# Kernel optimization log

Measured on AMD Instinct MI355X. Metric: run time of the kernel, lower is better.

Reference implementation:

```python
import jax, jax.numpy as jnp
import numpy as np

B, COND_LEN, E = 128, 256, 512   # batch, cond_len, hidden_dim (== conditioning_dim)
A, L, H = 128, 64, 8             # action_dim, num_action_steps, num_heads
STEPS = 20
HD = E // H


def setup_inputs() -> dict:
    key = jax.random.key(0)
    ks = jax.random.split(key, 16)
    def rn(k, shape, s=0.02):
        return jax.random.normal(k, shape, jnp.float32) * s
    return {
        "conditioning": jax.random.normal(ks[0], (B, COND_LEN, E), jnp.float32),
        "noise": jax.random.normal(ks[1], (B, L, A), jnp.float32),
        # time_embed: Linear(1,E) -> ReLU -> Linear(E,E)
        "t1_w": rn(ks[2], (E, 1)), "t1_b": jnp.zeros((E,), jnp.float32),
        "t2_w": rn(ks[3], (E, E)), "t2_b": jnp.zeros((E,), jnp.float32),
        # query_proj: Linear(A, E)
        "qp_w": rn(ks[4], (E, A)), "qp_b": jnp.zeros((E,), jnp.float32),
        # MultiheadAttention packed in_proj (3E, E) and out_proj (E, E)
        "in_w": rn(ks[5], (3 * E, E)), "in_b": jnp.zeros((3 * E,), jnp.float32),
        "op_w": rn(ks[6], (E, E)), "op_b": jnp.zeros((E,), jnp.float32),
        # output_proj: Linear(E, A)
        "outp_w": rn(ks[7], (A, E)), "outp_b": jnp.zeros((A,), jnp.float32),
        # ffn: Linear(A, 4A) -> ReLU -> Linear(4A, A)
        "f1_w": rn(ks[8], (4 * A, A)), "f1_b": jnp.zeros((4 * A,), jnp.float32),
        "f2_w": rn(ks[9], (A, 4 * A)), "f2_b": jnp.zeros((A,), jnp.float32),
        # LayerNorm(A)
        "ln_g": jnp.ones((A,), jnp.float32), "ln_b": jnp.zeros((A,), jnp.float32),
    }


def reference(conditioning, noise, t1_w, t1_b, t2_w, t2_b, qp_w, qp_b,
              in_w, in_b, op_w, op_b, outp_w, outp_b,
              f1_w, f1_b, f2_w, f2_b, ln_g, ln_b):
    dt = -1.0 / STEPS
    scale = 1.0 / np.sqrt(HD)
    # K/V of cross-attn depend only on conditioning -> hoist out of the loop
    # (same math as recomputing per step).
    k = (conditioning @ in_w[E:2 * E].T + in_b[E:2 * E]).reshape(B, COND_LEN, H, HD)
    v = (conditioning @ in_w[2 * E:].T + in_b[2 * E:]).reshape(B, COND_LEN, H, HD)

    def denoise(x_t, time):
        t = time[:, None]                                            # (B,1)
        t_emb = jnp.maximum(t @ t1_w.T + t1_b, 0.0) @ t2_w.T + t2_b  # (B,E)
        q_in = x_t @ qp_w.T + qp_b + t_emb[:, None, :]               # (B,L,E)
        q = (q_in @ in_w[:E].T + in_b[:E]).reshape(B, L, H, HD)
        scores = jnp.einsum('bqhd,bkhd->bhqk', q * scale, k)         # (B,H,L,COND_LEN)
        attn = jax.nn.softmax(scores, axis=-1)
        ctx = jnp.einsum('bhqk,bkhd->bqhd', attn, v).reshape(B, L, E)
        ctx = ctx @ op_w.T + op_b                                    # MHA out_proj
        v_t = ctx @ outp_w.T + outp_b                                # (B,L,A)
        h = x_t + v_t
        mu = jnp.mean(h, axis=-1, keepdims=True)
        var = jnp.mean((h - mu) ** 2, axis=-1, keepdims=True)
        hn = (h - mu) / jnp.sqrt(var + 1e-5) * ln_g + ln_b
        return hn + (jnp.maximum(hn @ f1_w.T + f1_b, 0.0) @ f2_w.T + f2_b)

    def step(carry, _):
        x_t, time = carry
        v_t = denoise(x_t, time)
        return (x_t + dt * v_t, time + dt), None

    init = (noise, jnp.ones((B,), jnp.float32))
    (x_t, _), _ = jax.lax.scan(step, init, None, length=STEPS)
    return x_t
```

## Files before the change

### kernel.cpp

```cpp
#include <hip/hip_runtime.h>

#define NB 128
#define CL 256
#define EE 512
#define AA 128
#define LL 64
#define HH 8
#define HD 64
#define NSTEPS 20
#define BLROWS (NB*LL)
#define LOG2E 1.4426950408889634f
#define QSCALE 64.0f
#define INV_QS 0.015625f

typedef __attribute__((ext_vector_type(8))) short bf16x8;
typedef __attribute__((ext_vector_type(4))) float f32x4;
typedef unsigned int u32;

union F8 { u32 u[2]; long l; };

__device__ __forceinline__ unsigned short f2bf(float f) {
    union { float f; unsigned u; } x; x.f = f;
    unsigned u = x.u;
    u += 0x7fffu + ((u >> 16) & 1u);
    return (unsigned short)(u >> 16);
}
__device__ __forceinline__ u32 pk4f8(f32x4 v) {
    u32 r = __builtin_amdgcn_cvt_pk_fp8_f32(v[0], v[1], 0, false);
    r = __builtin_amdgcn_cvt_pk_fp8_f32(v[2], v[3], r, true);
    return r;
}
__device__ __forceinline__ unsigned char f2f8(float v) {
    return (unsigned char)(__builtin_amdgcn_cvt_pk_fp8_f32(v, v, 0, false) & 0xffu);
}

__device__ __forceinline__ void async_copy16(const unsigned short* g, unsigned short* l) {
    __builtin_amdgcn_global_load_lds((const __attribute__((address_space(1))) u32*)g,
                                     (__attribute__((address_space(3))) u32*)l, 16, 0, 0);
}

#define MFMA(a,b,c)  __builtin_amdgcn_mfma_f32_16x16x32_bf16(a, b, c, 0, 0, 0)
#define MFMA8(a,b,c) __builtin_amdgcn_mfma_f32_16x16x32_fp8_fp8(a, b, c, 0, 0, 0)

__device__ __forceinline__ F8 build8(const u32* p, int kk, int srcA, int srcB, int odd) {
    u32 a0 = __shfl((int)p[2*kk],   srcA, 64);
    u32 b0 = __shfl((int)p[2*kk+1], srcA, 64);
    u32 a1 = __shfl((int)p[2*kk],   srcB, 64);
    u32 b1 = __shfl((int)p[2*kk+1], srcB, 64);
    F8 f; f.u[0] = odd ? b0 : a0; f.u[1] = odd ? b1 : a1;
    return f;
}


__global__ void cvt8_kernel(const float* __restrict__ src, unsigned short* __restrict__ dst, int n8) {
    int i = blockIdx.x*256 + threadIdx.x;
    if (i >= n8) return;
    const float* s = src + (size_t)i*8;
    f32x4 v0 = *(const f32x4*)s;
    f32x4 v1 = *(const f32x4*)(s + 4);
    bf16x8 o;
    o[0]=(short)f2bf(v0[0]); o[1]=(short)f2bf(v0[1]);
    o[2]=(short)f2bf(v0[2]); o[3]=(short)f2bf(v0[3]);
    o[4]=(short)f2bf(v1[0]); o[5]=(short)f2bf(v1[1]);
    o[6]=(short)f2bf(v1[2]); o[7]=(short)f2bf(v1[3]);
    *(bf16x8*)(dst + (size_t)i*8) = o;
}

__global__ void prep_eff_kernel(const float* __restrict__ in_w, const float* __restrict__ qp_w,
                                const float* __restrict__ outp_w, const float* __restrict__ op_w,
                                const float* __restrict__ op_b, const float* __restrict__ outp_b,
                                unsigned short* __restrict__ wq, unsigned short* __restrict__ wo,
                                float* __restrict__ bo) {
    int tid = blockIdx.x*256 + threadIdx.x;
    if (tid < 65536) {
        int n = tid >> 7, k = tid & 127;
        float s = 0.f;
        for (int e = 0; e < 512; ++e) s += in_w[(size_t)n*512 + e] * qp_w[(size_t)e*128 + k];
        wq[(size_t)n*128 + k] = f2bf(s * (0.125f * LOG2E * QSCALE));
    } else if (tid < 131072) {
        int t2 = tid - 65536; int n = t2 >> 9, k = t2 & 511;
        float s = 0.f;
        for (int e = 0; e < 512; ++e) s += outp_w[(size_t)n*512 + e] * op_w[(size_t)e*512 + k];
        wo[(size_t)n*512 + k] = f2bf(s);
    } else if (tid < 131200) {
        int n = tid - 131072;
        float s = outp_b[n];
        for (int e = 0; e < 512; ++e) s += outp_w[(size_t)n*512 + e] * op_b[e];
        bo[n] = s;
    }
}

__global__ void temb_kernel(const float* __restrict__ t1_w, const float* __restrict__ t1_b,
                            const float* __restrict__ t2_w, const float* __restrict__ t2_b,
                            float* __restrict__ temb) {
    int tid = blockIdx.x*256 + threadIdx.x;
    if (tid >= NSTEPS*512) return;
    int s = tid >> 9, e = tid & 511;
    float t = 1.0f - 0.05f * (float)s;
    float acc = t2_b[e];
    for (int i = 0; i < 512; ++i)
        acc += t2_w[(size_t)e*512 + i] * fmaxf(t * t1_w[i] + t1_b[i], 0.f);
    temb[tid] = acc;
}

__global__ void qbias_kernel(const float* __restrict__ in_w, const float* __restrict__ in_b,
                             const float* __restrict__ qp_b, const float* __restrict__ temb,
                             float* __restrict__ qbias) {
    int tid = blockIdx.x*256 + threadIdx.x;
    if (tid >= NSTEPS*512) return;
    int s = tid >> 9, n = tid & 511;
    float acc = in_b[n];
    const float* te = temb + (size_t)s*512;
    for (int e = 0; e < 512; ++e)
        acc += in_w[(size_t)n*512 + e] * (qp_b[e] + te[e]);
    qbias[tid] = acc * (0.125f * LOG2E * QSCALE);
}

__global__ __launch_bounds__(512, 8) void kv_kernel(const unsigned short* __restrict__ condb,
                                                    const unsigned short* __restrict__ wkv,
                                                    const float* __restrict__ bias,
                                                    unsigned char* __restrict__ K8,
                                                    unsigned char* __restrict__ V8) {
    __shared__ unsigned short As[128*64];
    __shared__ unsigned short Bs[128*64];
    int tid = threadIdx.x;
    int blk = blockIdx.x;
    int xcd = blk & 7, j = blk >> 3;
    int m0 = (xcd*32 + (j >> 3)) * 128;
    int n0 = (j & 7) * 128;
    int wv = tid >> 6, lane = tid & 63, r = lane & 15, q = lane >> 4;
    int srow = lane >> 3;
    int sg = (lane & 7) ^ srow;
    const unsigned short* agl = condb + (size_t)(m0 + wv*16 + srow)*512 + sg*8;
    const unsigned short* bgl = wkv   + (size_t)(n0 + wv*16 + srow)*512 + sg*8;
    f32x4 acc[8] = {};
#pragma unroll
    for (int kt = 0; kt < 8; ++kt) {
        int k0 = kt * 64;
#pragma unroll
        for (int ii = 0; ii < 2; ++ii) {
            async_copy16(agl + (size_t)(ii*8)*512 + k0, &As[(wv*16 + ii*8)*64]);
            async_copy16(bgl + (size_t)(ii*8)*512 + k0, &Bs[(wv*16 + ii*8)*64]);
        }
        __syncthreads();
#pragma unroll
        for (int kk = 0; kk < 2; ++kk) {
            int gof = ((kk*4 + q) ^ (r & 7)) * 8;
            bf16x8 a = *(const bf16x8*)&As[(wv*16 + r)*64 + gof];
#pragma unroll
            for (int t = 0; t < 8; ++t) {
                bf16x8 b = *(const bf16x8*)&Bs[(t*16 + r)*64 + gof];
                acc[t] = MFMA(a, b, acc[t]);
            }
        }
        __syncthreads();
    }
    int mbase = m0 + wv*16 + q*4;
    int bb = mbase >> 8, kpb = mbase & 255;
#pragma unroll
    for (int t = 0; t < 8; ++t) {
        int n = n0 + t*16 + r;
        float bs = bias[n];
        if (n < 512) {
            int h = n >> 6, d = n & 63;
            int colp = ((d>>3)&3)*16 + ((d>>5)&1)*8 + (d&7);
            unsigned char* kp = K8 + (size_t)(bb*HH + h)*16384 + colp;
#pragma unroll
            for (int i = 0; i < 4; ++i)
                kp[(kpb + i)*64] = f2f8(acc[t][i] + bs);
        } else {
            int n2 = n - 512, h = n2 >> 6, d = n2 & 63;
            int kk = kpb >> 5, qq = (kpb >> 3) & 3, jb = kpb & 7;
            int colv = (kk>>1)*64 + qq*16 + (kk&1)*8 + jb;
            u32 w01 = __builtin_amdgcn_cvt_pk_fp8_f32(acc[t][0]+bs, acc[t][1]+bs, 0, false);
            w01 = __builtin_amdgcn_cvt_pk_fp8_f32(acc[t][2]+bs, acc[t][3]+bs, w01, true);
            *(u32*)(V8 + (size_t)(bb*HH + h)*16384 + d*256 + colv) = w01;
        }
    }
}

__global__ __launch_bounds__(256, 2) void mega_kernel(
        const unsigned char* __restrict__ Kg,
        const unsigned char* __restrict__ Vg,
        const float* __restrict__ noise,
        const unsigned short* __restrict__ wq,
        const float* __restrict__ qbiasB,
        const unsigned short* __restrict__ wo,
        const float* __restrict__ bo,
        const float* __restrict__ ln_g, const float* __restrict__ ln_b,
        const unsigned short* __restrict__ f1w,
        const float* __restrict__ f1_b,
        const unsigned short* __restrict__ f2w,
        const float* __restrict__ f2_b,
        float* __restrict__ outp) {
    __shared__ unsigned short xS[16*136];
    __shared__ unsigned short cuS[16*520];
    __shared__ unsigned short hnS[16*136];
    __shared__ float redS[16*4], redS2[16*4];

    int tid = threadIdx.x, w = tid >> 6, lane = tid & 63, r = lane & 15, q = lane >> 4;
    int vblk = ((blockIdx.x & 7) << 6) | (blockIdx.x >> 3);
    int b = vblk >> 2;
    int row0 = vblk * 16;
    int srcA = r + ((2*q) & 3)*16;
    int srcB = r + ((2*q + 1) & 3)*16;
    int odd = (q >> 1) & 1;

    float xf[2][4];
#pragma unroll
    for (int t = 0; t < 2; ++t)
#pragma unroll
        for (int i = 0; i < 4; ++i) {
            int rl = q*4 + i, col = w*32 + t*16 + r;
            float v = noise[(size_t)(row0 + rl)*AA + col];
            xf[t][i] = v;
            xS[rl*136 + col] = f2bf(v);
        }
    __syncthreads();

    const float dt = -1.f / (float)NSTEPS;

#pragma unroll 1
    for (int s = 0; s < NSTEPS; ++s) {
        const float* qb_s = qbiasB + (size_t)s*512;

#pragma unroll 1
        for (int hp = 0; hp < 2; ++hp) {
            int h = w*2 + hp;
            const unsigned char* kbase = Kg + ((size_t)b*HH + h)*16384;
            const unsigned char* vbase = Vg + ((size_t)b*HH + h)*16384;

            f32x4 qacc[4] = {};
#pragma unroll
            for (int kk = 0; kk < 4; ++kk) {
                bf16x8 bx = *(const bf16x8*)&xS[(r)*136 + kk*32 + q*8];
#pragma unroll
                for (int t = 0; t < 4; ++t) {
                    bf16x8 a = *(const bf16x8*)(wq + (size_t)(h*HD + t*16 + r)*AA + kk*32 + q*8);
                    qacc[t] = MFMA(a, bx, qacc[t]);
                }
            }
            u32 qp[4];
#pragma unroll
            for (int t = 0; t < 4; ++t) {
                f32x4 qb4 = *(const f32x4*)(qb_s + h*HD + t*16 + q*4);
                f32x4 v;
#pragma unroll
                for (int i = 0; i < 4; ++i) v[i] = qacc[t][i] + qb4[i];
                qp[t] = pk4f8(v);
            }
            F8 bq[2];
            bq[0] = build8(qp, 0, srcA, srcB, odd);
            bq[1] = build8(qp, 1, srcA, srcB, odd);

            float mr = -3e38f, l = 0.f;
            f32x4 c[4] = {};

#pragma unroll
            for (int qq = 0; qq < 4; ++qq) {
                uint4 kbuf[4];
#pragma unroll
                for (int t = 0; t < 4; ++t)
                    kbuf[t] = *(const uint4*)(kbase + (size_t)((qq*4 + t)*16 + r)*64 + q*16);

                f32x4 s0[4] = {};
#pragma unroll
                for (int t = 0; t < 4; ++t) {
                    F8 k0, k1;
                    k0.u[0] = kbuf[t].x; k0.u[1] = kbuf[t].y;
                    k1.u[0] = kbuf[t].z; k1.u[1] = kbuf[t].w;
                    s0[t] = MFMA8(k0.l, bq[0].l, s0[t]);
                    s0[t] = MFMA8(k1.l, bq[1].l, s0[t]);
                }

                uint4 vbuf[4];
#pragma unroll
                for (int t = 0; t < 4; ++t)
                    vbuf[t] = *(const uint4*)(vbase + (size_t)(t*16 + r)*256 + qq*64 + q*16);

                float a0 = s0[0][0], a1 = s0[0][1], a2 = s0[0][2], a3 = s0[0][3];
#pragma unroll
                for (int t = 1; t < 4; ++t) {
                    a0 = fmaxf(a0, s0[t][0]); a1 = fmaxf(a1, s0[t][1]);
                    a2 = fmaxf(a2, s0[t][2]); a3 = fmaxf(a3, s0[t][3]);
                }
                float hm = fmaxf(fmaxf(a0, a1), fmaxf(a2, a3));
                hm = fmaxf(hm, __shfl_xor(hm, 16));
                hm = fmaxf(hm, __shfl_xor(hm, 32));
                float nm = fmaxf(mr, hm * INV_QS);
                float rs = exp2f(mr - nm);
                mr = nm;

                u32 pp[4];
                float t00 = 0.f, t01 = 0.f;
#pragma unroll
                for (int t = 0; t < 4; ++t) {
                    float e0 = exp2f(fmaf(s0[t][0], INV_QS, -nm));
                    float e1 = exp2f(fmaf(s0[t][1], INV_QS, -nm));
                    float e2 = exp2f(fmaf(s0[t][2], INV_QS, -nm));
                    float e3 = exp2f(fmaf(s0[t][3], INV_QS, -nm));
                    t00 += e0 + e2; t01 += e1 + e3;
                    f32x4 w0; w0[0]=e0*QSCALE; w0[1]=e1*QSCALE; w0[2]=e2*QSCALE; w0[3]=e3*QSCALE;
                    pp[t] = pk4f8(w0);
                }
                l = l * rs + (t00 + t01);

                float rr[4];
#pragma unroll
                for (int i = 0; i < 4; ++i) rr[i] = __shfl(rs, q*4 + i);
#pragma unroll
                for (int t = 0; t < 4; ++t)
#pragma unroll
                    for (int i = 0; i < 4; ++i) c[t][i] *= rr[i];

                {
                    F8 a0f = build8(pp, 0, srcA, srcB, odd);
                    F8 a1f = build8(pp, 1, srcA, srcB, odd);
#pragma unroll
                    for (int t = 0; t < 4; ++t) {
                        F8 v0, v1;
                        v0.u[0] = vbuf[t].x; v0.u[1] = vbuf[t].y;
                        v1.u[0] = vbuf[t].z; v1.u[1] = vbuf[t].w;
                        c[t] = MFMA8(a0f.l, v0.l, c[t]);
                        c[t] = MFMA8(a1f.l, v1.l, c[t]);
                    }
                }
            }

            l += __shfl_xor(l, 16); l += __shfl_xor(l, 32);
            float iv = 1.0f / l;
            float sc[4];
#pragma unroll
            for (int i = 0; i < 4; ++i) sc[i] = INV_QS * __shfl(iv, q*4 + i);
#pragma unroll
            for (int t = 0; t < 4; ++t)
#pragma unroll
                for (int i = 0; i < 4; ++i)
                    cuS[(q*4 + i)*520 + h*HD + t*16 + r] = f2bf(c[t][i] * sc[i]);
        }
        __syncthreads();

        f32x4 oacc[2] = {};
#pragma unroll
        for (int kk = 0; kk < 16; ++kk) {
            bf16x8 a = *(const bf16x8*)&cuS[(r)*520 + kk*32 + q*8];
#pragma unroll
            for (int t = 0; t < 2; ++t) {
                bf16x8 bw = *(const bf16x8*)(wo + (size_t)(w*32 + t*16 + r)*EE + kk*32 + q*8);
                oacc[t] = MFMA(a, bw, oacc[t]);
            }
        }
        float hv[2][4];
#pragma unroll
        for (int t = 0; t < 2; ++t) {
            float bov = bo[w*32 + t*16 + r];
#pragma unroll
            for (int i = 0; i < 4; ++i) hv[t][i] = oacc[t][i] + bov + xf[t][i];
        }
#pragma unroll
        for (int i = 0; i < 4; ++i) {
            float s1 = hv[0][i] + hv[1][i];
            float s2 = hv[0][i]*hv[0][i] + hv[1][i]*hv[1][i];
            s1 += __shfl_xor(s1, 1);  s2 += __shfl_xor(s2, 1);
            s1 += __shfl_xor(s1, 2);  s2 += __shfl_xor(s2, 2);
            s1 += __shfl_xor(s1, 4);  s2 += __shfl_xor(s2, 4);
            s1 += __shfl_xor(s1, 8);  s2 += __shfl_xor(s2, 8);
            if (r == 0) { redS[(q*4 + i)*4 + w] = s1; redS2[(q*4 + i)*4 + w] = s2; }
        }
        __syncthreads();
        float hnv[2][4];
#pragma unroll
        for (int i = 0; i < 4; ++i) {
            int row = q*4 + i;
            float s1 = redS [row*4+0] + redS [row*4+1] + redS [row*4+2] + redS [row*4+3];
            float s2 = redS2[row*4+0] + redS2[row*4+1] + redS2[row*4+2] + redS2[row*4+3];
            float mu = s1 * (1.f/128.f);
            float var = s2 * (1.f/128.f) - mu*mu;
            float rstd = rsqrtf(var + 1e-5f);
#pragma unroll
            for (int t = 0; t < 2; ++t) {
                int col = w*32 + t*16 + r;
                float v = (hv[t][i] - mu) * rstd * ln_g[col] + ln_b[col];
                hnv[t][i] = v;
                hnS[row*136 + col] = f2bf(v);
            }
        }
        __syncthreads();

        f32x4 o2[2] = {};
#pragma unroll 1
        for (int nt = 0; nt < 4; ++nt) {
            f32x4 a1[2] = {};
#pragma unroll
            for (int kk = 0; kk < 4; ++kk) {
                bf16x8 a = *(const bf16x8*)&hnS[(r)*136 + kk*32 + q*8];
#pragma unroll
                for (int t = 0; t < 2; ++t) {
                    bf16x8 bw = *(const bf16x8*)(f1w + (size_t)(nt*128 + w*32 + t*16 + r)*AA + kk*32 + q*8);
                    a1[t] = MFMA(a, bw, a1[t]);
                }
            }
#pragma unroll
            for (int t = 0; t < 2; ++t) {
                float b1 = f1_b[nt*128 + w*32 + t*16 + r];
#pragma unroll
                for (int i = 0; i < 4; ++i)
                    cuS[(q*4 + i)*520 + nt*128 + w*32 + t*16 + r] = f2bf(fmaxf(a1[t][i] + b1, 0.f));
            }
        }
        __syncthreads();
#pragma unroll 1
        for (int nt = 0; nt < 4; ++nt) {
#pragma unroll
            for (int kk = 0; kk < 4; ++kk) {
                bf16x8 a = *(const bf16x8*)&cuS[(r)*520 + nt*128 + kk*32 + q*8];
#pragma unroll
                for (int t = 0; t < 2; ++t) {
                    bf16x8 bw = *(const bf16x8*)(f2w + (size_t)(w*32 + t*16 + r)*EE + nt*128 + kk*32 + q*8);
                    o2[t] = MFMA(a, bw, o2[t]);
                }
            }
        }

        if (s < NSTEPS - 1) {
#pragma unroll
            for (int t = 0; t < 2; ++t) {
                float b2 = f2_b[w*32 + t*16 + r];
#pragma unroll
                for (int i = 0; i < 4; ++i) {
                    float outv = hnv[t][i] + o2[t][i] + b2;
                    float xn = xf[t][i] + dt * outv;
                    xf[t][i] = xn;
                    xS[(q*4 + i)*136 + w*32 + t*16 + r] = f2bf(xn);
                }
            }
            __syncthreads();
        } else {
#pragma unroll
            for (int t = 0; t < 2; ++t) {
                float b2 = f2_b[w*32 + t*16 + r];
#pragma unroll
                for (int i = 0; i < 4; ++i) {
                    float outv = hnv[t][i] + o2[t][i] + b2;
                    outp[(size_t)(row0 + q*4 + i)*AA + w*32 + t*16 + r] = xf[t][i] + dt * outv;
                }
            }
        }
    }
}

extern "C" void kernel_launch(void* const* d_in, const int* in_sizes, int n_in,
                              void* d_out, int out_size, void* d_ws, size_t ws_size,
                              hipStream_t stream) {
    const float* cond   = (const float*)d_in[0];
    const float* noise  = (const float*)d_in[1];
    const float* t1_w   = (const float*)d_in[2];
    const float* t1_b   = (const float*)d_in[3];
    const float* t2_w   = (const float*)d_in[4];
    const float* t2_b   = (const float*)d_in[5];
    const float* qp_w   = (const float*)d_in[6];
    const float* qp_b   = (const float*)d_in[7];
    const float* in_w   = (const float*)d_in[8];
    const float* in_b   = (const float*)d_in[9];
    const float* op_w   = (const float*)d_in[10];
    const float* op_b   = (const float*)d_in[11];
    const float* outp_w = (const float*)d_in[12];
    const float* outp_b = (const float*)d_in[13];
    const float* f1_w   = (const float*)d_in[14];
    const float* f1_b   = (const float*)d_in[15];
    const float* f2_w   = (const float*)d_in[16];
    const float* f2_b   = (const float*)d_in[17];
    const float* ln_g   = (const float*)d_in[18];
    const float* ln_bp  = (const float*)d_in[19];

    char* w = (char*)d_ws;
    auto alloc = [&](size_t bytes) {
        char* p = w;
        w += (bytes + 255) & ~(size_t)255;
        return p;
    };
    unsigned char*  K8     = (unsigned char*)alloc((size_t)NB*HH*CL*HD);
    unsigned char*  V8     = (unsigned char*)alloc((size_t)NB*HH*HD*CL);
    unsigned short* condb  = (unsigned short*)alloc((size_t)NB*CL*EE*2);
    unsigned short* wkv_bf = (unsigned short*)alloc((size_t)1024*512*2);
    unsigned short* wq_bf  = (unsigned short*)alloc((size_t)512*128*2);
    unsigned short* wo_bf  = (unsigned short*)alloc((size_t)128*512*2);
    unsigned short* f1_bf  = (unsigned short*)alloc((size_t)512*128*2);
    unsigned short* f2_bf  = (unsigned short*)alloc((size_t)128*512*2);
    float*          bo_eff = (float*)alloc(128*4);
    float*          tembB  = (float*)alloc((size_t)NSTEPS*512*4);
    float*          qbiasB = (float*)alloc((size_t)NSTEPS*512*4);
    (void)ws_size; (void)n_in; (void)in_sizes; (void)out_size;

    cvt8_kernel<<<8192, 256, 0, stream>>>(cond, condb, NB*CL*EE/8);
    cvt8_kernel<<<256, 256, 0, stream>>>(in_w + 512*512, wkv_bf, 1024*512/8);
    cvt8_kernel<<<32, 256, 0, stream>>>(f1_w, f1_bf, 512*128/8);
    cvt8_kernel<<<32, 256, 0, stream>>>(f2_w, f2_bf, 128*512/8);
    prep_eff_kernel<<<513, 256, 0, stream>>>(in_w, qp_w, outp_w, op_w, op_b, outp_b,
                                             wq_bf, wo_bf, bo_eff);
    temb_kernel<<<40, 256, 0, stream>>>(t1_w, t1_b, t2_w, t2_b, tembB);
    qbias_kernel<<<40, 256, 0, stream>>>(in_w, in_b, qp_b, tembB, qbiasB);
    kv_kernel<<<2048, 512, 0, stream>>>(condb, wkv_bf, in_b + 512, K8, V8);

    mega_kernel<<<512, 256, 0, stream>>>(K8, V8, noise, wq_bf, qbiasB,
                                         wo_bf, bo_eff, ln_g, ln_bp,
                                         f1_bf, f1_b, f2_bf, f2_b,
                                         (float*)d_out);
}
```

Baseline: 1.109 ms.

## Replace online softmax with single-pass full-row softmax in cross-attention

Rather than processing the 256 conditioning keys in four chunks with an online-softmax rescale, the kernel now loads all K tiles, computes all 16 score tiles, does one max/exp/sum pass, then runs the PV MFMAs. This drops the per-chunk max reduction shuffles, the running rescale of the accumulator and its exp2, and lets all K and V loads be issued up front. In exchange, register pressure rises (16 uint4 K and V buffers plus 16 f32x4 score accumulators), which could lower occupancy or cause spills.

After: 1.238 ms. 1.12x slower.

```diff
diff --git a/kernel.cpp b/kernel.cpp
--- a/kernel.cpp
+++ b/kernel.cpp
@@ -49,6 +49,38 @@
     u32 b1 = __shfl((int)p[2*kk+1], srcB, 64);
     F8 f; f.u[0] = odd ? b0 : a0; f.u[1] = odd ? b1 : a1;
     return f;
+}
+
+__device__ __forceinline__ float softmax8v(const f32x4* sacc, u32* pp8) {
+    float mx0 = sacc[0][0], mx1 = sacc[0][1], mx2 = sacc[0][2], mx3 = sacc[0][3];
+#pragma unroll
+    for (int t = 1; t < 16; ++t) {
+        mx0 = fmaxf(mx0, sacc[t][0]);
+        mx1 = fmaxf(mx1, sacc[t][1]);
+        mx2 = fmaxf(mx2, sacc[t][2]);
+        mx3 = fmaxf(mx3, sacc[t][3]);
+    }
+    float mx = fmaxf(fmaxf(mx0, mx1), fmaxf(mx2, mx3));
+    mx = fmaxf(mx, __shfl_xor(mx, 16));
+    mx = fmaxf(mx, __shfl_xor(mx, 32));
+    float mxc = mx * INV_QS;
+    float s0 = 0.f, s1 = 0.f, s2 = 0.f, s3 = 0.f;
+#pragma unroll
+    for (int t = 0; t < 16; ++t) {
+        float e0 = exp2f(fmaf(sacc[t][0], INV_QS, -mxc));
+        float e1 = exp2f(fmaf(sacc[t][1], INV_QS, -mxc));
+        float e2 = exp2f(fmaf(sacc[t][2], INV_QS, -mxc));
+        float e3 = exp2f(fmaf(sacc[t][3], INV_QS, -mxc));
+        s0 += e0; s1 += e1; s2 += e2; s3 += e3;
+        f32x4 w;
+        w[0] = e0 * QSCALE; w[1] = e1 * QSCALE;
+        w[2] = e2 * QSCALE; w[3] = e3 * QSCALE;
+        pp8[t] = pk4f8(w);
+    }
+    float sum = (s0 + s1) + (s2 + s3);
+    sum += __shfl_xor(sum, 16);
+    sum += __shfl_xor(sum, 32);
+    return 1.0f / sum;
 }
 
 
@@ -253,82 +285,44 @@
             bq[0] = build8(qp, 0, srcA, srcB, odd);
             bq[1] = build8(qp, 1, srcA, srcB, odd);
 
-            float mr = -3e38f, l = 0.f;
+            uint4 kbuf[16];
+#pragma unroll
+            for (int t = 0; t < 16; ++t)
+                kbuf[t] = *(const uint4*)(kbase + (size_t)(t*16 + r)*64 + q*16);
+            f32x4 sacc[16] = {};
+#pragma unroll
+            for (int t = 0; t < 16; ++t) {
+                F8 k0, k1;
+                k0.u[0] = kbuf[t].x; k0.u[1] = kbuf[t].y;
+                k1.u[0] = kbuf[t].z; k1.u[1] = kbuf[t].w;
+                sacc[t] = MFMA8(k0.l, bq[0].l, sacc[t]);
+                sacc[t] = MFMA8(k1.l, bq[1].l, sacc[t]);
+            }
+
+            uint4 vbuf[16];
+#pragma unroll
+            for (int kp = 0; kp < 4; ++kp)
+#pragma unroll
+                for (int t = 0; t < 4; ++t)
+                    vbuf[kp*4 + t] = *(const uint4*)(vbase + (size_t)(t*16 + r)*256 + kp*64 + q*16);
+
+            u32 pp[16];
+            float iv = softmax8v(sacc, pp);
+
             f32x4 c[4] = {};
-
-#pragma unroll
-            for (int qq = 0; qq < 4; ++qq) {
-                uint4 kbuf[4];
-#pragma unroll
-                for (int t = 0; t < 4; ++t)
-                    kbuf[t] = *(const uint4*)(kbase + (size_t)((qq*4 + t)*16 + r)*64 + q*16);
-
-                f32x4 s0[4] = {};
+#pragma unroll
+            for (int kp = 0; kp < 4; ++kp) {
+                F8 a0f = build8(pp, 2*kp,   srcA, srcB, odd);
+                F8 a1f = build8(pp, 2*kp+1, srcA, srcB, odd);
 #pragma unroll
                 for (int t = 0; t < 4; ++t) {
-                    F8 k0, k1;
-                    k0.u[0] = kbuf[t].x; k0.u[1] = kbuf[t].y;
-                    k1.u[0] = kbuf[t].z; k1.u[1] = kbuf[t].w;
-                    s0[t] = MFMA8(k0.l, bq[0].l, s0[t]);
-                    s0[t] = MFMA8(k1.l, bq[1].l, s0[t]);
+                    F8 v0, v1;
+                    v0.u[0] = vbuf[kp*4+t].x; v0.u[1] = vbuf[kp*4+t].y;
+                    v1.u[0] = vbuf[kp*4+t].z; v1.u[1] = vbuf[kp*4+t].w;
+                    c[t] = MFMA8(a0f.l, v0.l, c[t]);
+                    c[t] = MFMA8(a1f.l, v1.l, c[t]);
                 }
-
-                uint4 vbuf[4];
-#pragma unroll
-                for (int t = 0; t < 4; ++t)
-                    vbuf[t] = *(const uint4*)(vbase + (size_t)(t*16 + r)*256 + qq*64 + q*16);
-
-                float a0 = s0[0][0], a1 = s0[0][1], a2 = s0[0][2], a3 = s0[0][3];
-#pragma unroll
-                for (int t = 1; t < 4; ++t) {
-                    a0 = fmaxf(a0, s0[t][0]); a1 = fmaxf(a1, s0[t][1]);
-                    a2 = fmaxf(a2, s0[t][2]); a3 = fmaxf(a3, s0[t][3]);
-                }
-                float hm = fmaxf(fmaxf(a0, a1), fmaxf(a2, a3));
-                hm = fmaxf(hm, __shfl_xor(hm, 16));
-                hm = fmaxf(hm, __shfl_xor(hm, 32));
-                float nm = fmaxf(mr, hm * INV_QS);
-                float rs = exp2f(mr - nm);
-                mr = nm;
-
-                u32 pp[4];
-                float t00 = 0.f, t01 = 0.f;
-#pragma unroll
-                for (int t = 0; t < 4; ++t) {
-                    float e0 = exp2f(fmaf(s0[t][0], INV_QS, -nm));
-                    float e1 = exp2f(fmaf(s0[t][1], INV_QS, -nm));
-                    float e2 = exp2f(fmaf(s0[t][2], INV_QS, -nm));
-                    float e3 = exp2f(fmaf(s0[t][3], INV_QS, -nm));
-                    t00 += e0 + e2; t01 += e1 + e3;
-                    f32x4 w0; w0[0]=e0*QSCALE; w0[1]=e1*QSCALE; w0[2]=e2*QSCALE; w0[3]=e3*QSCALE;
-                    pp[t] = pk4f8(w0);
-                }
-                l = l * rs + (t00 + t01);
-
-                float rr[4];
-#pragma unroll
-                for (int i = 0; i < 4; ++i) rr[i] = __shfl(rs, q*4 + i);
-#pragma unroll
-                for (int t = 0; t < 4; ++t)
-#pragma unroll
-                    for (int i = 0; i < 4; ++i) c[t][i] *= rr[i];
-
-                {
-                    F8 a0f = build8(pp, 0, srcA, srcB, odd);
-                    F8 a1f = build8(pp, 1, srcA, srcB, odd);
-#pragma unroll
-                    for (int t = 0; t < 4; ++t) {
-                        F8 v0, v1;
-                        v0.u[0] = vbuf[t].x; v0.u[1] = vbuf[t].y;
-                        v1.u[0] = vbuf[t].z; v1.u[1] = vbuf[t].w;
-                        c[t] = MFMA8(a0f.l, v0.l, c[t]);
-                        c[t] = MFMA8(a1f.l, v1.l, c[t]);
-                    }
-                }
-            }
-
-            l += __shfl_xor(l, 16); l += __shfl_xor(l, 32);
-            float iv = 1.0f / l;
+            }
             float sc[4];
 #pragma unroll
             for (int i = 0; i < 4; ++i) sc[i] = INV_QS * __shfl(iv, q*4 + i);
```
